# Performance work log

Hardware: AMD Instinct MI355X
Metric: run time of the kernel (lower is better)

The kernel has to match this reference:

```python
import jax, jax.numpy as jnp
import numpy as np
import math

B, T, N, D = 4, 12, 1024, 64
LN_EPS = 1e-5


def setup_inputs() -> dict:
    key = jax.random.key(0)
    k1, k2, k3 = jax.random.split(key, 3)
    X = jax.random.normal(k1, (B, T, N, D), dtype=jnp.float32)
    A = jax.random.uniform(k2, (N, N), dtype=jnp.float32)
    W = jax.random.normal(k3, (D, D), dtype=jnp.float32) * (1.0 / math.sqrt(D))
    gamma = jnp.ones((D,), dtype=jnp.float32)
    beta = jnp.zeros((D,), dtype=jnp.float32)
    return {"X": X, "A": A, "W": W, "gamma": gamma, "beta": beta}


def reference(X, A, W, gamma, beta):
    d = X.shape[-1]
    # dynamic attention scores: (b,t,n,m)
    scores = jnp.einsum('btnd,btmd->btnm', X, X)
    St = jax.nn.softmax(scores, axis=-1) / jnp.sqrt(jnp.float32(d)) + 1e-8
    # adjacency-gated dynamic graph: A (n,m) broadcast over (b,t)
    Ag = A[None, None, :, :] * St
    # graph conv: aggregate then linear (nn.Linear: H @ W.T), relu
    H = jnp.einsum('btnm,btmd->btnd', Ag, X)
    out = jax.nn.relu(H @ W.T)
    # layernorm over last dim
    mu = jnp.mean(out, axis=-1, keepdims=True)
    var = jnp.var(out, axis=-1, keepdims=True)
    out = (out - mu) * jax.lax.rsqrt(var + LN_EPS) * gamma + beta
    # residual
    return out + X
```

## Files before the change

kernel.cpp:

```cpp
#include <hip/hip_runtime.h>
#include <hip/hip_bf16.h>
#include <math.h>


typedef short bf16x8 __attribute__((ext_vector_type(8)));
typedef float f32x4  __attribute__((ext_vector_type(4)));
typedef float f32x16 __attribute__((ext_vector_type(16)));
typedef int   i32x4  __attribute__((ext_vector_type(4)));

constexpr int kN = 1024;
constexpr int kD = 64;
constexpr size_t kPlane    = 48u * 1024u * 64u;
constexpr size_t kAfShorts = 16u * 32u * 2048u;
constexpr float  kLog2e    = 1.4426950408889634f;

#define MFMA32(a,b,c) __builtin_amdgcn_mfma_f32_32x32x16_bf16((a),(b),(c),0,0,0)
#define MFMA16(a,b,c) __builtin_amdgcn_mfma_f32_16x16x32_bf16((a),(b),(c),0,0,0)

__device__ __forceinline__ void splitv(float v, short& h, short& l) {
  unsigned u = __float_as_uint(v);
  h = (short)(u >> 16);
  float hf = __uint_as_float(u & 0xFFFF0000u);
  l = (short)(__float_as_uint(v - hf) >> 16);
}

__device__ __forceinline__ short rndbf(float v) {
  unsigned u = __float_as_uint(v);
  return (short)((u + 0x7FFFu + ((u >> 16) & 1u)) >> 16);
}

__device__ __forceinline__ unsigned pkbf(float a, float b) {
  return (__float_as_uint(a) >> 16) | (__float_as_uint(b) & 0xFFFF0000u);
}

__global__ __launch_bounds__(256)
void presplit(const float* __restrict__ X, short* __restrict__ Xh,
              short* __restrict__ XTh)
{
  __shared__ short Sh[64][68];
  const int t  = threadIdx.x;
  const int bt = blockIdx.x >> 4;
  const int mb = blockIdx.x & 15;
  const size_t base = (size_t)bt * 65536 + (size_t)mb * 64 * 64;

#pragma unroll
  for (int k = 0; k < 4; ++k) {
    int idx = t + k * 256;
    int row = idx >> 4;
    int c4  = (idx & 15) * 4;
    float4 v = *(const float4*)(X + base + row * 64 + c4);
    short4 hv = make_short4(rndbf(v.x), rndbf(v.y), rndbf(v.z), rndbf(v.w));
    *(short4*)(Xh + base + row * 64 + c4) = hv;
    *(short4*)&Sh[row][c4] = hv;
  }
  __syncthreads();

  const size_t tbase = (size_t)bt * 65536 + (size_t)mb * 64;
#pragma unroll
  for (int k = 0; k < 2; ++k) {
    int idx = t + k * 256;
    int d   = idx >> 3;
    int m8  = (idx & 7) * 8;
    bf16x8 hv;
#pragma unroll
    for (int j = 0; j < 8; ++j) hv[j] = Sh[m8 + j][d];
    *(bf16x8*)(XTh + tbase + (size_t)d * 1024 + m8) = hv;
  }
}

__global__ __launch_bounds__(256)
void prearr_Abf(const float* __restrict__ A, short* __restrict__ Af)
{
  const int qt  = blockIdx.x >> 5;
  const int gks = blockIdx.x & 31;
  const int kb  = gks * 32;
  const int s   = threadIdx.x;
  short* dst = Af + ((size_t)(qt * 32 + gks) * 2048);

  const int qw = s >> 7;
  const int ln = (s >> 1) & 63;
  const int p  = s & 1;
  const int q  = qt * 64 + qw * 32 + (ln & 31);
  const int h  = ln >> 5;
  const int k0 = kb + 16 * p + 4 * h;
  float4 f0 = *(const float4*)(A + (size_t)q * kN + k0);
  float4 f1 = *(const float4*)(A + (size_t)q * kN + k0 + 8);
  i32x4 u;
  u[0] = (int)pkbf(f0.x, f0.y); u[1] = (int)pkbf(f0.z, f0.w);
  u[2] = (int)pkbf(f1.x, f1.y); u[3] = (int)pkbf(f1.z, f1.w);
  *(i32x4*)(dst + (size_t)qw * 1024 + ln * 16 + p * 8) = u;
}

template<int AMODE>
__global__ __launch_bounds__(256)
void sdgcn_v15(const float* __restrict__ X, const float* __restrict__ A,
               const float* __restrict__ W, const float* __restrict__ gamma,
               const float* __restrict__ beta, float* __restrict__ out,
               const short* __restrict__ Xh, const short* __restrict__ XTh,
               const short* __restrict__ Af)
{
  __shared__ __align__(16) unsigned char LB[38912];

  const int t    = threadIdx.x;
  const int wave = t >> 6;
  const int lane = t & 63;
  const int kg   = wave >> 1;
  const int qw   = wave & 1;
  const int half = lane >> 5;
  const int l31  = lane & 31;
  const int bid  = blockIdx.x;
  const int swz  = (bid & 7) * 96 + (bid >> 3);
  const int bt   = swz >> 4;
  const int qt   = swz & 15;
  const int qblk = qt * 64;
  const size_t xb = (size_t)bt * 65536;

  short* Kh0 = (short*)(LB + kg * 4608);
  short* Kh1 = (short*)(LB + 9216 + kg * 4608);
  short* Vt0 = (short*)(LB + 18432 + kg * 5120);
  short* Vt1 = (short*)(LB + 28672 + kg * 5120);
  float* aM  = (float*)LB;
  float* aZ  = aM + 128;
  float* aF  = aZ + 128;
  float* Har = (float*)(LB + 1792);

  const int qmine = qblk + qw * 32 + l31;
  bf16x8 qh[4];
#pragma unroll
  for (int c = 0; c < 4; ++c)
    qh[c] = *(const bf16x8*)(Xh + xb + (size_t)qmine * kD + 16 * c + half * 8);

  f32x16 o0, o1;
#pragma unroll
  for (int r = 0; r < 16; ++r) { o0[r] = 0.f; o1[r] = 0.f; }
  float mrun = -INFINITY, Z = 0.f;

  const int tg = t & 127;

  auto ldK = [&](int kb, int j, bf16x8& h) {
    int ck = tg + 128 * j; int kr = ck >> 3; int kc = (ck & 7) * 8;
    h = *(const bf16x8*)(Xh + xb + (size_t)(kb + kr) * kD + kc);
  };
  auto ldV = [&](int kb, int j, bf16x8& h) {
    int cv = tg + 128 * j; int vd = cv >> 2; int vm = (cv & 3) * 8;
    h = *(const bf16x8*)(XTh + xb + (size_t)vd * 1024 + kb + vm);
  };
  auto stK = [&](short* Kh, int j, bf16x8 h) {
    int ck = tg + 128 * j; int kr = ck >> 3; int kc = (ck & 7) * 8;
    *(bf16x8*)&Kh[kr * 72 + kc] = h;
  };
  auto stV = [&](short* Vt, int j, bf16x8 h) {
    int cv = tg + 128 * j; int vd = cv >> 2; int vm = (cv & 3) * 8;
    *(bf16x8*)&Vt[vd * 40 + vm] = h;
  };

  i32x4 aA = {0,0,0,0}, aB = {0,0,0,0};

  auto compute = [&](int ks, const short* Khg, const short* Vtg, bool pfA) {
    const int kb = kg * 512 + ks * 32;

    i32x4 naA = {0,0,0,0}, naB = {0,0,0,0};
    if (AMODE == 1 && pfA) {
      const short* Ab = Af + ((size_t)(qt * 32 + kg * 16 + ks + 1) * 2048)
                           + (size_t)qw * 1024 + (lane << 4);
      naA = *(const i32x4*)(Ab);
      naB = *(const i32x4*)(Ab + 8);
    }

    float agv[16];
    if (AMODE == 1) {
      unsigned u[8] = {(unsigned)aA[0],(unsigned)aA[1],(unsigned)aA[2],(unsigned)aA[3],
                       (unsigned)aB[0],(unsigned)aB[1],(unsigned)aB[2],(unsigned)aB[3]};
#pragma unroll
      for (int m = 0; m < 8; ++m) {
        agv[2*m]   = __uint_as_float(u[m] << 16);
        agv[2*m+1] = __uint_as_float(u[m] & 0xFFFF0000u);
      }
    } else {
      const float* Arow = A + (size_t)qmine * kN + kb + 4 * half;
      float4 ag0 = *(const float4*)(Arow);
      float4 ag1 = *(const float4*)(Arow + 8);
      float4 ag2 = *(const float4*)(Arow + 16);
      float4 ag3 = *(const float4*)(Arow + 24);
#pragma unroll
      for (int e = 0; e < 4; ++e) {
        agv[e] = ag0[e]; agv[4+e] = ag1[e]; agv[8+e] = ag2[e]; agv[12+e] = ag3[e];
      }
    }

    f32x16 sa;
#pragma unroll
    for (int r = 0; r < 16; ++r) sa[r] = 0.f;
    __builtin_amdgcn_s_setprio(1);
#pragma unroll
    for (int c = 0; c < 4; ++c) {
      bf16x8 kh = *(const bf16x8*)&Khg[l31 * 72 + 16 * c + half * 8];
      sa = MFMA32(kh, qh[c], sa);
    }
    __builtin_amdgcn_s_setprio(0);

    float a0 = fmaxf(fmaxf(sa[0],  sa[1]),  sa[2]);
    float a1 = fmaxf(fmaxf(sa[3],  sa[4]),  sa[5]);
    float a2 = fmaxf(fmaxf(sa[6],  sa[7]),  sa[8]);
    float a3 = fmaxf(fmaxf(sa[9],  sa[10]), sa[11]);
    float a4 = fmaxf(fmaxf(sa[12], sa[13]), sa[14]);
    float b0 = fmaxf(fmaxf(a0, a1), a2);
    float sm = fmaxf(fmaxf(b0, fmaxf(a3, a4)), sa[15]);
    sm = fmaxf(sm, __shfl_xor(sm, 32, 64));
    if (__any(sm > mrun + 8.f)) {
      const float nm = fmaxf(mrun, sm);
      const float f  = exp2f((mrun - nm) * kLog2e);
      mrun = nm; Z *= f;
#pragma unroll
      for (int r = 0; r < 16; ++r) {
        const float fr = __shfl(f, (r & 3) + 8 * (r >> 2) + 4 * half, 64);
        o0[r] *= fr; o1[r] *= fr;
      }
    }
    const float mb2 = mrun * kLog2e;
    float pv[16];
#pragma unroll
    for (int r = 0; r < 16; ++r) pv[r] = exp2f(fmaf(sa[r], kLog2e, -mb2));
    float z0 = (pv[0] + pv[1]) + (pv[2] + pv[3]);
    float z1 = (pv[4] + pv[5]) + (pv[6] + pv[7]);
    float z2 = (pv[8] + pv[9]) + (pv[10] + pv[11]);
    float z3 = (pv[12] + pv[13]) + (pv[14] + pv[15]);
    float zt = (z0 + z1) + (z2 + z3);
    zt += __shfl_xor(zt, 32, 64);
    Z += zt;

    float pa[16];
#pragma unroll
    for (int r = 0; r < 16; ++r) pa[r] = pv[r] * agv[r];

    unsigned du[8];
#pragma unroll
    for (int j = 0; j < 8; ++j) du[j] = pkbf(pa[2*j], pa[2*j+1]);
    const bool lo = (half == 0);
    unsigned snd0 = lo ? du[2] : du[0];
    unsigned snd1 = lo ? du[3] : du[1];
    unsigned snd2 = lo ? du[6] : du[4];
    unsigned snd3 = lo ? du[7] : du[5];
    unsigned r0 = (unsigned)__shfl_xor((int)snd0, 32, 64);
    unsigned r1 = (unsigned)__shfl_xor((int)snd1, 32, 64);
    unsigned r2 = (unsigned)__shfl_xor((int)snd2, 32, 64);
    unsigned r3 = (unsigned)__shfl_xor((int)snd3, 32, 64);
    i32x4 w0, w1;
    w0[0] = (int)(lo ? du[0] : r0);
    w0[1] = (int)(lo ? du[1] : r1);
    w0[2] = (int)(lo ? r0 : du[2]);
    w0[3] = (int)(lo ? r1 : du[3]);
    w1[0] = (int)(lo ? du[4] : r2);
    w1[1] = (int)(lo ? du[5] : r3);
    w1[2] = (int)(lo ? r2 : du[6]);
    w1[3] = (int)(lo ? r3 : du[7]);
    bf16x8 pf0 = *(bf16x8*)&w0;
    bf16x8 pf1 = *(bf16x8*)&w1;

    {
      bf16x8 v0 = *(const bf16x8*)&Vtg[l31 * 40 + half * 8];
      bf16x8 v1 = *(const bf16x8*)&Vtg[l31 * 40 + 16 + half * 8];
      bf16x8 v2 = *(const bf16x8*)&Vtg[(32 + l31) * 40 + half * 8];
      bf16x8 v3 = *(const bf16x8*)&Vtg[(32 + l31) * 40 + 16 + half * 8];
      __builtin_amdgcn_s_setprio(1);
      o0 = MFMA32(pf0, v0, o0);
      o0 = MFMA32(pf1, v1, o0);
      o1 = MFMA32(pf0, v2, o1);
      o1 = MFMA32(pf1, v3, o1);
      __builtin_amdgcn_s_setprio(0);
    }
    aA = naA; aB = naB;
  };

  {
    bf16x8 a0,b0,c0,d0;
    ldK(kg * 512, 0, a0); ldK(kg * 512, 1, b0);
    ldV(kg * 512, 0, c0); ldV(kg * 512, 1, d0);
    stK(Kh0, 0, a0); stK(Kh0, 1, b0); stV(Vt0, 0, c0); stV(Vt0, 1, d0);
  }
  if (AMODE == 1) {
    const short* Ab = Af + ((size_t)(qt * 32 + kg * 16) * 2048)
                         + (size_t)qw * 1024 + (lane << 4);
    aA = *(const i32x4*)(Ab);
    aB = *(const i32x4*)(Ab + 8);
  }
  __syncthreads();

  for (int ks = 0; ks < 16; ks += 2) {
    bf16x8 k0,k1,v0,v1;
    ldK(kg * 512 + (ks + 1) * 32, 0, k0);
    ldK(kg * 512 + (ks + 1) * 32, 1, k1);
    ldV(kg * 512 + (ks + 1) * 32, 0, v0);
    ldV(kg * 512 + (ks + 1) * 32, 1, v1);
    compute(ks, Kh0, Vt0, true);
    stK(Kh1, 0, k0); stK(Kh1, 1, k1); stV(Vt1, 0, v0); stV(Vt1, 1, v1);
    __syncthreads();

    const bool more = (ks + 2) < 16;
    if (more) {
      ldK(kg * 512 + (ks + 2) * 32, 0, k0);
      ldK(kg * 512 + (ks + 2) * 32, 1, k1);
      ldV(kg * 512 + (ks + 2) * 32, 0, v0);
      ldV(kg * 512 + (ks + 2) * 32, 1, v1);
    }
    compute(ks + 1, Kh1, Vt1, more);
    if (more) {
      stK(Kh0, 0, k0); stK(Kh0, 1, k1); stV(Vt0, 0, v0); stV(Vt0, 1, v1);
    }
    __syncthreads();
  }

  if (lane < 32) {
    aM[kg * 64 + qw * 32 + l31] = mrun;
    aZ[kg * 64 + qw * 32 + l31] = Z;
  }
  if (kg == 1) {
#pragma unroll
    for (int r = 0; r < 16; ++r) {
      const int qq = qw * 32 + (r & 3) + 8 * (r >> 2) + 4 * half;
      Har[qq * 68 + l31]      = o0[r];
      Har[qq * 68 + l31 + 32] = o1[r];
    }
  }
  __syncthreads();
  if (kg == 1 && lane < 32) {
    const int q = qw * 32 + l31;
    const float ma = aM[q], mb = mrun;
    const float m  = fmaxf(ma, mb);
    const float fa = __expf(ma - m), fb = __expf(mb - m);
    const float Zs = aZ[q] * fa + Z * fb;
    aF[q]       = fa;
    aF[64 + q]  = fb;
    aF[128 + q] = 1.0f / (8.0f * Zs);
  }
  __syncthreads();
  if (kg == 0) {
#pragma unroll
    for (int r = 0; r < 16; ++r) {
      const int qq = qw * 32 + (r & 3) + 8 * (r >> 2) + 4 * half;
      const float fa = aF[qq], fb = aF[64 + qq];
      Har[qq * 68 + l31]      = o0[r] * fa + Har[qq * 68 + l31]      * fb;
      Har[qq * 68 + l31 + 32] = o1[r] * fa + Har[qq * 68 + l31 + 32] * fb;
    }
  }
  __syncthreads();

  const int g  = lane >> 4;
  const int ql = lane & 15;
  const int er = wave * 16;
  const float i8z = aF[128 + er + ql];

  bf16x8 hh[2], hl[2];
#pragma unroll
  for (int kk = 0; kk < 2; ++kk) {
    const float* hp = &Har[(er + ql) * 68 + kk * 32 + g * 8];
    float4 v0 = *(const float4*)hp;
    float4 v1 = *(const float4*)(hp + 4);
    float v[8] = {v0.x*i8z, v0.y*i8z, v0.z*i8z, v0.w*i8z,
                  v1.x*i8z, v1.y*i8z, v1.z*i8z, v1.w*i8z};
#pragma unroll
    for (int e = 0; e < 8; ++e) { short a, b; splitv(v[e], a, b); hh[kk][e] = a; hl[kk][e] = b; }
  }

  f32x4 lin[4];
#pragma unroll
  for (int c = 0; c < 4; ++c) {
    bf16x8 wh[2], wl[2];
#pragma unroll
    for (int kk = 0; kk < 2; ++kk) {
      const float* wp = W + (size_t)(c * 16 + ql) * kD + kk * 32 + g * 8;
      float4 v0 = *(const float4*)wp;
      float4 v1 = *(const float4*)(wp + 4);
      float v[8] = {v0.x, v0.y, v0.z, v0.w, v1.x, v1.y, v1.z, v1.w};
#pragma unroll
      for (int e = 0; e < 8; ++e) { short a, b; splitv(v[e], a, b); wh[kk][e] = a; wl[kk][e] = b; }
    }
    f32x4 acc = {0.f, 0.f, 0.f, 0.f};
    acc = MFMA16(hh[0], wh[0], acc);
    acc = MFMA16(hh[1], wh[1], acc);
    acc = MFMA16(hh[0], wl[0], acc);
    acc = MFMA16(hh[1], wl[1], acc);
    acc = MFMA16(hl[0], wh[0], acc);
    acc = MFMA16(hl[1], wh[1], acc);
    lin[c] = acc;
  }

  float rl[4][4];
#pragma unroll
  for (int c = 0; c < 4; ++c)
#pragma unroll
    for (int r = 0; r < 4; ++r) rl[c][r] = fmaxf(lin[c][r], 0.f);

  float mu[4], rstd[4];
#pragma unroll
  for (int r = 0; r < 4; ++r) {
    float s1 = rl[0][r] + rl[1][r] + rl[2][r] + rl[3][r];
    float s2 = rl[0][r]*rl[0][r] + rl[1][r]*rl[1][r] + rl[2][r]*rl[2][r] + rl[3][r]*rl[3][r];
#pragma unroll
    for (int off = 1; off < 16; off <<= 1) {
      s1 += __shfl_xor(s1, off, 64);
      s2 += __shfl_xor(s2, off, 64);
    }
    mu[r] = s1 * (1.f / 64.f);
    const float var = s2 * (1.f / 64.f) - mu[r] * mu[r];
    rstd[r] = rsqrtf(var + 1e-5f);
  }

#pragma unroll
  for (int c = 0; c < 4; ++c) {
    const float gm = gamma[c * 16 + ql];
    const float bb = beta[c * 16 + ql];
#pragma unroll
    for (int r = 0; r < 4; ++r) {
      const int qrow = qblk + er + 4 * g + r;
      const size_t off = ((size_t)bt * kN + qrow) * kD + c * 16 + ql;
      out[off] = (rl[c][r] - mu[r]) * rstd[r] * gm + bb + X[off];
    }
  }
}

extern "C" void kernel_launch(void* const* d_in, const int* in_sizes, int n_in,
                              void* d_out, int out_size, void* d_ws, size_t ws_size,
                              hipStream_t stream) {
  const float* X     = (const float*)d_in[0];
  const float* A     = (const float*)d_in[1];
  const float* W     = (const float*)d_in[2];
  const float* gamma = (const float*)d_in[3];
  const float* beta  = (const float*)d_in[4];
  float* out = (float*)d_out;

  short* Xh  = (short*)d_ws;
  short* XTh = Xh  + kPlane;
  short* Af  = XTh + kPlane;

  const size_t need = (2 * kPlane + kAfShorts) * sizeof(short);

  presplit<<<dim3(48 * 16), 256, 0, stream>>>(X, Xh, XTh);
  if (ws_size >= need) {
    prearr_Abf<<<dim3(16 * 32), 256, 0, stream>>>(A, Af);
    sdgcn_v15<1><<<dim3(48 * 16), 256, 0, stream>>>(X, A, W, gamma, beta, out,
                                                    Xh, XTh, Af);
  } else {
    sdgcn_v15<0><<<dim3(48 * 16), 256, 0, stream>>>(X, A, W, gamma, beta, out,
                                                    Xh, XTh, Af);
  }
}
```

Baseline: 63.65 us.

## Software-pipeline QK^T one tile ahead of softmax and PV with triple-buffered V

Restructures the main loop so the QK^T MFMAs for tile ts+1 run before the softmax and PV for tile ts, keeping the previous scores in registers. K stays double-buffered, V moves to a triple buffer, and global loads are issued two tiles ahead. The aim is to overlap MFMA work with the exp/shuffle softmax math and global latency, and to have one barrier per tile instead of per-half-pair. The cost is more LDS (48KB), which may reduce occupancy, plus extra register pressure from a second live score accumulator.

```diff
diff --git a/kernel.cpp b/kernel.cpp
--- a/kernel.cpp
+++ b/kernel.cpp
@@ -93,13 +93,13 @@
 
 template<int AMODE>
 __global__ __launch_bounds__(256)
-void sdgcn_v15(const float* __restrict__ X, const float* __restrict__ A,
+void sdgcn_v17(const float* __restrict__ X, const float* __restrict__ A,
                const float* __restrict__ W, const float* __restrict__ gamma,
                const float* __restrict__ beta, float* __restrict__ out,
                const short* __restrict__ Xh, const short* __restrict__ XTh,
                const short* __restrict__ Af)
 {
-  __shared__ __align__(16) unsigned char LB[38912];
+  __shared__ __align__(16) unsigned char LB[49152];
 
   const int t    = threadIdx.x;
   const int wave = t >> 6;
@@ -115,10 +115,11 @@
   const int qblk = qt * 64;
   const size_t xb = (size_t)bt * 65536;
 
-  short* Kh0 = (short*)(LB + kg * 4608);
-  short* Kh1 = (short*)(LB + 9216 + kg * 4608);
-  short* Vt0 = (short*)(LB + 18432 + kg * 5120);
-  short* Vt1 = (short*)(LB + 28672 + kg * 5120);
+  short* Kb0 = (short*)(LB + kg * 4608);
+  short* Kb1 = (short*)(LB + 9216 + kg * 4608);
+  short* Vb0 = (short*)(LB + 18432 + kg * 5120);
+  short* Vb1 = (short*)(LB + 28672 + kg * 5120);
+  short* Vb2 = (short*)(LB + 38912 + kg * 5120);
   float* aM  = (float*)LB;
   float* aZ  = aM + 128;
   float* aF  = aZ + 128;
@@ -154,14 +155,64 @@
     *(bf16x8*)&Vt[vd * 40 + vm] = h;
   };
 
+  auto QK = [&](const short* Khg, f32x16& sa) {
+#pragma unroll
+    for (int r = 0; r < 16; ++r) sa[r] = 0.f;
+    __builtin_amdgcn_s_setprio(1);
+#pragma unroll
+    for (int c = 0; c < 4; ++c) {
+      bf16x8 kh = *(const bf16x8*)&Khg[l31 * 72 + 16 * c + half * 8];
+      sa = MFMA32(kh, qh[c], sa);
+    }
+    __builtin_amdgcn_s_setprio(0);
+  };
+
   i32x4 aA = {0,0,0,0}, aB = {0,0,0,0};
 
-  auto compute = [&](int ks, const short* Khg, const short* Vtg, bool pfA) {
-    const int kb = kg * 512 + ks * 32;
-
+  {
+    bf16x8 a0,b0,c0,d0;
+    ldK(kg * 512, 0, a0); ldK(kg * 512, 1, b0);
+    ldV(kg * 512, 0, c0); ldV(kg * 512, 1, d0);
+    stK(Kb0, 0, a0); stK(Kb0, 1, b0); stV(Vb0, 0, c0); stV(Vb0, 1, d0);
+  }
+  if (AMODE == 1) {
+    const short* Ab = Af + ((size_t)(qt * 32 + kg * 16) * 2048)
+                         + (size_t)qw * 1024 + (lane << 4);
+    aA = *(const i32x4*)(Ab);
+    aB = *(const i32x4*)(Ab + 8);
+  }
+  __syncthreads();
+
+  f32x16 sa_prev;
+  QK(Kb0, sa_prev);
+  {
+    bf16x8 a0,b0,c0,d0;
+    ldK(kg * 512 + 32, 0, a0); ldK(kg * 512 + 32, 1, b0);
+    ldV(kg * 512 + 32, 0, c0); ldV(kg * 512 + 32, 1, d0);
+    stK(Kb1, 0, a0); stK(Kb1, 1, b0); stV(Vb1, 0, c0); stV(Vb1, 1, d0);
+  }
+
+  short* k_rd = Kb1;
+  short* k_wr = Kb0;
+  short* v_rd = Vb0;
+  short* v_rot = Vb1;
+  short* v_w2 = Vb2;
+
+  for (int ts = 0; ts < 16; ++ts) {
+    __syncthreads();
+
+    f32x16 sa_new;
+    if (ts < 15) QK(k_rd, sa_new);
+
+    bf16x8 nk0, nk1, nv0, nv1;
+    if (ts < 14) {
+      const int kb2 = kg * 512 + (ts + 2) * 32;
+      ldK(kb2, 0, nk0); ldK(kb2, 1, nk1);
+      ldV(kb2, 0, nv0); ldV(kb2, 1, nv1);
+    }
     i32x4 naA = {0,0,0,0}, naB = {0,0,0,0};
-    if (AMODE == 1 && pfA) {
-      const short* Ab = Af + ((size_t)(qt * 32 + kg * 16 + ks + 1) * 2048)
+    if (AMODE == 1 && ts < 15) {
+      const short* Ab = Af + ((size_t)(qt * 32 + kg * 16 + ts + 1) * 2048)
                            + (size_t)qw * 1024 + (lane << 4);
       naA = *(const i32x4*)(Ab);
       naB = *(const i32x4*)(Ab + 8);
@@ -177,7 +228,7 @@
         agv[2*m+1] = __uint_as_float(u[m] & 0xFFFF0000u);
       }
     } else {
-      const float* Arow = A + (size_t)qmine * kN + kb + 4 * half;
+      const float* Arow = A + (size_t)qmine * kN + kg * 512 + ts * 32 + 4 * half;
       float4 ag0 = *(const float4*)(Arow);
       float4 ag1 = *(const float4*)(Arow + 8);
       float4 ag2 = *(const float4*)(Arow + 16);
@@ -188,24 +239,13 @@
       }
     }
 
-    f32x16 sa;
-#pragma unroll
-    for (int r = 0; r < 16; ++r) sa[r] = 0.f;
-    __builtin_amdgcn_s_setprio(1);
-#pragma unroll
-    for (int c = 0; c < 4; ++c) {
-      bf16x8 kh = *(const bf16x8*)&Khg[l31 * 72 + 16 * c + half * 8];
-      sa = MFMA32(kh, qh[c], sa);
-    }
-    __builtin_amdgcn_s_setprio(0);
-
-    float a0 = fmaxf(fmaxf(sa[0],  sa[1]),  sa[2]);
-    float a1 = fmaxf(fmaxf(sa[3],  sa[4]),  sa[5]);
-    float a2 = fmaxf(fmaxf(sa[6],  sa[7]),  sa[8]);
-    float a3 = fmaxf(fmaxf(sa[9],  sa[10]), sa[11]);
-    float a4 = fmaxf(fmaxf(sa[12], sa[13]), sa[14]);
+    float a0 = fmaxf(fmaxf(sa_prev[0],  sa_prev[1]),  sa_prev[2]);
+    float a1 = fmaxf(fmaxf(sa_prev[3],  sa_prev[4]),  sa_prev[5]);
+    float a2 = fmaxf(fmaxf(sa_prev[6],  sa_prev[7]),  sa_prev[8]);
+    float a3 = fmaxf(fmaxf(sa_prev[9],  sa_prev[10]), sa_prev[11]);
+    float a4 = fmaxf(fmaxf(sa_prev[12], sa_prev[13]), sa_prev[14]);
     float b0 = fmaxf(fmaxf(a0, a1), a2);
-    float sm = fmaxf(fmaxf(b0, fmaxf(a3, a4)), sa[15]);
+    float sm = fmaxf(fmaxf(b0, fmaxf(a3, a4)), sa_prev[15]);
     sm = fmaxf(sm, __shfl_xor(sm, 32, 64));
     if (__any(sm > mrun + 8.f)) {
       const float nm = fmaxf(mrun, sm);
@@ -220,7 +260,7 @@
     const float mb2 = mrun * kLog2e;
     float pv[16];
 #pragma unroll
-    for (int r = 0; r < 16; ++r) pv[r] = exp2f(fmaf(sa[r], kLog2e, -mb2));
+    for (int r = 0; r < 16; ++r) pv[r] = exp2f(fmaf(sa_prev[r], kLog2e, -mb2));
     float z0 = (pv[0] + pv[1]) + (pv[2] + pv[3]);
     float z1 = (pv[4] + pv[5]) + (pv[6] + pv[7]);
     float z2 = (pv[8] + pv[9]) + (pv[10] + pv[11]);
@@ -258,10 +298,10 @@
     bf16x8 pf1 = *(bf16x8*)&w1;
 
     {
-      bf16x8 v0 = *(const bf16x8*)&Vtg[l31 * 40 + half * 8];
-      bf16x8 v1 = *(const bf16x8*)&Vtg[l31 * 40 + 16 + half * 8];
-      bf16x8 v2 = *(const bf16x8*)&Vtg[(32 + l31) * 40 + half * 8];
-      bf16x8 v3 = *(const bf16x8*)&Vtg[(32 + l31) * 40 + 16 + half * 8];
+      bf16x8 v0 = *(const bf16x8*)&v_rd[l31 * 40 + half * 8];
+      bf16x8 v1 = *(const bf16x8*)&v_rd[l31 * 40 + 16 + half * 8];
+      bf16x8 v2 = *(const bf16x8*)&v_rd[(32 + l31) * 40 + half * 8];
+      bf16x8 v3 = *(const bf16x8*)&v_rd[(32 + l31) * 40 + 16 + half * 8];
       __builtin_amdgcn_s_setprio(1);
       o0 = MFMA32(pf0, v0, o0);
       o0 = MFMA32(pf1, v1, o0);
@@ -269,46 +309,18 @@
       o1 = MFMA32(pf1, v3, o1);
       __builtin_amdgcn_s_setprio(0);
     }
+
+    if (ts < 14) {
+      stK(k_wr, 0, nk0); stK(k_wr, 1, nk1);
+      stV(v_w2, 0, nv0); stV(v_w2, 1, nv1);
+    }
+
+    { short* tmp = k_rd; k_rd = k_wr; k_wr = tmp; }
+    { short* tmp = v_rd; v_rd = v_rot; v_rot = v_w2; v_w2 = tmp; }
+    sa_prev = sa_new;
     aA = naA; aB = naB;
-  };
-
-  {
-    bf16x8 a0,b0,c0,d0;
-    ldK(kg * 512, 0, a0); ldK(kg * 512, 1, b0);
-    ldV(kg * 512, 0, c0); ldV(kg * 512, 1, d0);
-    stK(Kh0, 0, a0); stK(Kh0, 1, b0); stV(Vt0, 0, c0); stV(Vt0, 1, d0);
-  }
-  if (AMODE == 1) {
-    const short* Ab = Af + ((size_t)(qt * 32 + kg * 16) * 2048)
-                         + (size_t)qw * 1024 + (lane << 4);
-    aA = *(const i32x4*)(Ab);
-    aB = *(const i32x4*)(Ab + 8);
-  }
-  __syncthreads();
-
-  for (int ks = 0; ks < 16; ks += 2) {
-    bf16x8 k0,k1,v0,v1;
-    ldK(kg * 512 + (ks + 1) * 32, 0, k0);
-    ldK(kg * 512 + (ks + 1) * 32, 1, k1);
-    ldV(kg * 512 + (ks + 1) * 32, 0, v0);
-    ldV(kg * 512 + (ks + 1) * 32, 1, v1);
-    compute(ks, Kh0, Vt0, true);
-    stK(Kh1, 0, k0); stK(Kh1, 1, k1); stV(Vt1, 0, v0); stV(Vt1, 1, v1);
-    __syncthreads();
-
-    const bool more = (ks + 2) < 16;
-    if (more) {
-      ldK(kg * 512 + (ks + 2) * 32, 0, k0);
-      ldK(kg * 512 + (ks + 2) * 32, 1, k1);
-      ldV(kg * 512 + (ks + 2) * 32, 0, v0);
-      ldV(kg * 512 + (ks + 2) * 32, 1, v1);
-    }
-    compute(ks + 1, Kh1, Vt1, more);
-    if (more) {
-      stK(Kh0, 0, k0); stK(Kh0, 1, k1); stV(Vt0, 0, v0); stV(Vt0, 1, v1);
-    }
-    __syncthreads();
-  }
+  }
+  __syncthreads();
 
   if (lane < 32) {
     aM[kg * 64 + qw * 32 + l31] = mrun;
@@ -438,10 +450,10 @@
   presplit<<<dim3(48 * 16), 256, 0, stream>>>(X, Xh, XTh);
   if (ws_size >= need) {
     prearr_Abf<<<dim3(16 * 32), 256, 0, stream>>>(A, Af);
-    sdgcn_v15<1><<<dim3(48 * 16), 256, 0, stream>>>(X, A, W, gamma, beta, out,
+    sdgcn_v17<1><<<dim3(48 * 16), 256, 0, stream>>>(X, A, W, gamma, beta, out,
                                                     Xh, XTh, Af);
   } else {
-    sdgcn_v15<0><<<dim3(48 * 16), 256, 0, stream>>>(X, A, W, gamma, beta, out,
+    sdgcn_v17<0><<<dim3(48 * 16), 256, 0, stream>>>(X, A, W, gamma, beta, out,
                                                     Xh, XTh, Af);
   }
 }
```

Result: no change. 64.45 us (+1.3%).

## Give each wave a private LDS K/V tile and drop per-step block barriers

Applied to the files above, without the earlier changes.

Each wave now loads its own copy of the 32-key K and V^T tiles into a private LDS region, instead of two waves cooperatively filling shared double buffers. This removes the two __syncthreads per pair of key steps, so waves no longer stall on each other inside the main loop. In exchange, the two query waves in a key group fetch the same K/V data twice, doubling global/L2 load traffic. Each wave now uses a single LDS buffer, with the next tile's stores issued after the current step's LDS reads.

```diff
diff --git a/kernel.cpp b/kernel.cpp
--- a/kernel.cpp
+++ b/kernel.cpp
@@ -93,7 +93,7 @@
 
 template<int AMODE>
 __global__ __launch_bounds__(256)
-void sdgcn_v15(const float* __restrict__ X, const float* __restrict__ A,
+void sdgcn_v18(const float* __restrict__ X, const float* __restrict__ A,
                const float* __restrict__ W, const float* __restrict__ gamma,
                const float* __restrict__ beta, float* __restrict__ out,
                const short* __restrict__ Xh, const short* __restrict__ XTh,
@@ -115,10 +115,8 @@
   const int qblk = qt * 64;
   const size_t xb = (size_t)bt * 65536;
 
-  short* Kh0 = (short*)(LB + kg * 4608);
-  short* Kh1 = (short*)(LB + 9216 + kg * 4608);
-  short* Vt0 = (short*)(LB + 18432 + kg * 5120);
-  short* Vt1 = (short*)(LB + 28672 + kg * 5120);
+  short* Kw  = (short*)(LB + wave * 9728);
+  short* Vw  = (short*)(LB + wave * 9728 + 4608);
   float* aM  = (float*)LB;
   float* aZ  = aM + 128;
   float* aF  = aZ + 128;
@@ -135,33 +133,60 @@
   for (int r = 0; r < 16; ++r) { o0[r] = 0.f; o1[r] = 0.f; }
   float mrun = -INFINITY, Z = 0.f;
 
-  const int tg = t & 127;
-
-  auto ldK = [&](int kb, int j, bf16x8& h) {
-    int ck = tg + 128 * j; int kr = ck >> 3; int kc = (ck & 7) * 8;
-    h = *(const bf16x8*)(Xh + xb + (size_t)(kb + kr) * kD + kc);
+  auto ldK8 = [&](int kb, bf16x8 r[4]) {
+#pragma unroll
+    for (int j = 0; j < 4; ++j) {
+      int idx = lane + 64 * j;
+      int kr = idx >> 3, kc = (idx & 7) * 8;
+      r[j] = *(const bf16x8*)(Xh + xb + (size_t)(kb + kr) * kD + kc);
+    }
   };
-  auto ldV = [&](int kb, int j, bf16x8& h) {
-    int cv = tg + 128 * j; int vd = cv >> 2; int vm = (cv & 3) * 8;
-    h = *(const bf16x8*)(XTh + xb + (size_t)vd * 1024 + kb + vm);
+  auto stK8 = [&](const bf16x8 r[4]) {
+#pragma unroll
+    for (int j = 0; j < 4; ++j) {
+      int idx = lane + 64 * j;
+      *(bf16x8*)&Kw[(idx >> 3) * 72 + (idx & 7) * 8] = r[j];
+    }
   };
-  auto stK = [&](short* Kh, int j, bf16x8 h) {
-    int ck = tg + 128 * j; int kr = ck >> 3; int kc = (ck & 7) * 8;
-    *(bf16x8*)&Kh[kr * 72 + kc] = h;
+  auto ldV8 = [&](int kb, bf16x8 r[4]) {
+#pragma unroll
+    for (int j = 0; j < 4; ++j) {
+      int idx = lane + 64 * j;
+      int vd = idx >> 2, vm = (idx & 3) * 8;
+      r[j] = *(const bf16x8*)(XTh + xb + (size_t)vd * 1024 + kb + vm);
+    }
   };
-  auto stV = [&](short* Vt, int j, bf16x8 h) {
-    int cv = tg + 128 * j; int vd = cv >> 2; int vm = (cv & 3) * 8;
-    *(bf16x8*)&Vt[vd * 40 + vm] = h;
+  auto stV8 = [&](const bf16x8 r[4]) {
+#pragma unroll
+    for (int j = 0; j < 4; ++j) {
+      int idx = lane + 64 * j;
+      *(bf16x8*)&Vw[(idx >> 2) * 40 + (idx & 3) * 8] = r[j];
+    }
   };
 
   i32x4 aA = {0,0,0,0}, aB = {0,0,0,0};
 
-  auto compute = [&](int ks, const short* Khg, const short* Vtg, bool pfA) {
-    const int kb = kg * 512 + ks * 32;
-
+  {
+    bf16x8 kr4[4], vr4[4];
+    ldK8(kg * 512, kr4); ldV8(kg * 512, vr4);
+    stK8(kr4); stV8(vr4);
+  }
+  if (AMODE == 1) {
+    const short* Ab = Af + ((size_t)(qt * 32 + kg * 16) * 2048)
+                         + (size_t)qw * 1024 + (lane << 4);
+    aA = *(const i32x4*)(Ab);
+    aB = *(const i32x4*)(Ab + 8);
+  }
+
+  for (int ts = 0; ts < 16; ++ts) {
+    const int kb = kg * 512 + ts * 32;
+    const bool pfm = (ts + 1) < 16;
+
+    bf16x8 nk[4], nv[4];
+    if (pfm) { ldK8(kb + 32, nk); ldV8(kb + 32, nv); }
     i32x4 naA = {0,0,0,0}, naB = {0,0,0,0};
-    if (AMODE == 1 && pfA) {
-      const short* Ab = Af + ((size_t)(qt * 32 + kg * 16 + ks + 1) * 2048)
+    if (AMODE == 1 && pfm) {
+      const short* Ab = Af + ((size_t)(qt * 32 + kg * 16 + ts + 1) * 2048)
                            + (size_t)qw * 1024 + (lane << 4);
       naA = *(const i32x4*)(Ab);
       naB = *(const i32x4*)(Ab + 8);
@@ -194,7 +219,7 @@
     __builtin_amdgcn_s_setprio(1);
 #pragma unroll
     for (int c = 0; c < 4; ++c) {
-      bf16x8 kh = *(const bf16x8*)&Khg[l31 * 72 + 16 * c + half * 8];
+      bf16x8 kh = *(const bf16x8*)&Kw[l31 * 72 + 16 * c + half * 8];
       sa = MFMA32(kh, qh[c], sa);
     }
     __builtin_amdgcn_s_setprio(0);
@@ -258,10 +283,10 @@
     bf16x8 pf1 = *(bf16x8*)&w1;
 
     {
-      bf16x8 v0 = *(const bf16x8*)&Vtg[l31 * 40 + half * 8];
-      bf16x8 v1 = *(const bf16x8*)&Vtg[l31 * 40 + 16 + half * 8];
-      bf16x8 v2 = *(const bf16x8*)&Vtg[(32 + l31) * 40 + half * 8];
-      bf16x8 v3 = *(const bf16x8*)&Vtg[(32 + l31) * 40 + 16 + half * 8];
+      bf16x8 v0 = *(const bf16x8*)&Vw[l31 * 40 + half * 8];
+      bf16x8 v1 = *(const bf16x8*)&Vw[l31 * 40 + 16 + half * 8];
+      bf16x8 v2 = *(const bf16x8*)&Vw[(32 + l31) * 40 + half * 8];
+      bf16x8 v3 = *(const bf16x8*)&Vw[(32 + l31) * 40 + 16 + half * 8];
       __builtin_amdgcn_s_setprio(1);
       o0 = MFMA32(pf0, v0, o0);
       o0 = MFMA32(pf1, v1, o0);
@@ -269,46 +294,12 @@
       o1 = MFMA32(pf1, v3, o1);
       __builtin_amdgcn_s_setprio(0);
     }
+
+    if (pfm) { stK8(nk); stV8(nv); }
+
     aA = naA; aB = naB;
-  };
-
-  {
-    bf16x8 a0,b0,c0,d0;
-    ldK(kg * 512, 0, a0); ldK(kg * 512, 1, b0);
-    ldV(kg * 512, 0, c0); ldV(kg * 512, 1, d0);
-    stK(Kh0, 0, a0); stK(Kh0, 1, b0); stV(Vt0, 0, c0); stV(Vt0, 1, d0);
-  }
-  if (AMODE == 1) {
-    const short* Ab = Af + ((size_t)(qt * 32 + kg * 16) * 2048)
-                         + (size_t)qw * 1024 + (lane << 4);
-    aA = *(const i32x4*)(Ab);
-    aB = *(const i32x4*)(Ab + 8);
   }
   __syncthreads();
-
-  for (int ks = 0; ks < 16; ks += 2) {
-    bf16x8 k0,k1,v0,v1;
-    ldK(kg * 512 + (ks + 1) * 32, 0, k0);
-    ldK(kg * 512 + (ks + 1) * 32, 1, k1);
-    ldV(kg * 512 + (ks + 1) * 32, 0, v0);
-    ldV(kg * 512 + (ks + 1) * 32, 1, v1);
-    compute(ks, Kh0, Vt0, true);
-    stK(Kh1, 0, k0); stK(Kh1, 1, k1); stV(Vt1, 0, v0); stV(Vt1, 1, v1);
-    __syncthreads();
-
-    const bool more = (ks + 2) < 16;
-    if (more) {
-      ldK(kg * 512 + (ks + 2) * 32, 0, k0);
-      ldK(kg * 512 + (ks + 2) * 32, 1, k1);
-      ldV(kg * 512 + (ks + 2) * 32, 0, v0);
-      ldV(kg * 512 + (ks + 2) * 32, 1, v1);
-    }
-    compute(ks + 1, Kh1, Vt1, more);
-    if (more) {
-      stK(Kh0, 0, k0); stK(Kh0, 1, k1); stV(Vt0, 0, v0); stV(Vt0, 1, v1);
-    }
-    __syncthreads();
-  }
 
   if (lane < 32) {
     aM[kg * 64 + qw * 32 + l31] = mrun;
@@ -438,10 +429,10 @@
   presplit<<<dim3(48 * 16), 256, 0, stream>>>(X, Xh, XTh);
   if (ws_size >= need) {
     prearr_Abf<<<dim3(16 * 32), 256, 0, stream>>>(A, Af);
-    sdgcn_v15<1><<<dim3(48 * 16), 256, 0, stream>>>(X, A, W, gamma, beta, out,
+    sdgcn_v18<1><<<dim3(48 * 16), 256, 0, stream>>>(X, A, W, gamma, beta, out,
                                                     Xh, XTh, Af);
   } else {
-    sdgcn_v15<0><<<dim3(48 * 16), 256, 0, stream>>>(X, A, W, gamma, beta, out,
+    sdgcn_v18<0><<<dim3(48 * 16), 256, 0, stream>>>(X, A, W, gamma, beta, out,
                                                     Xh, XTh, Af);
   }
 }
```

Result: no change. 63.01 us (-1.0%).
